# Kernel optimization log

Measured on AMD Instinct MI355X. Metric: run time of the kernel, lower is better.

## Reference

```python
import jax, jax.numpy as jnp
import numpy as np

N, D, C, E = 100000, 128, 16, 1000000
NUM_LAYERS, ALPHA = 5, 0.5
EPS_COS, EPS_LN = 1e-8, 1e-5


def setup_inputs() -> dict:
    key = jax.random.key(0)
    ks = jax.random.split(key, 10)
    inp = {
        'features': jax.random.normal(ks[0], (N, D), jnp.float32),
        'init_logits': jax.random.uniform(ks[1], (N, C), jnp.float32),
        'W': jax.random.normal(ks[2], (D, D), jnp.float32) * (1.0 / np.sqrt(D)),
        'b': jnp.zeros((D,), jnp.float32),
        'ln_gamma': jnp.ones((D,), jnp.float32),
        'ln_beta': jnp.zeros((D,), jnp.float32),
        'ew_connect': jnp.ones((1,), jnp.float32),
        'ew_decorate': jnp.ones((1,), jnp.float32),
        'ew_next': jnp.ones((1,), jnp.float32),
    }
    names = ['src_connect', 'dst_connect', 'src_decorate', 'dst_decorate', 'src_next', 'dst_next']
    for i, nm in enumerate(names):
        inp[nm] = jax.random.randint(ks[4 + (i % 6)] if False else jax.random.fold_in(ks[3], i), (E,), 0, N, jnp.int32)
    return inp


def _label_prop(features, init_logits, W, b, ln_gamma, ln_beta, ews, edges):
    # feature_transform: Linear -> LayerNorm -> ReLU (Dropout is identity in eval)
    h = features @ W.T + b
    mu = jnp.mean(h, axis=-1, keepdims=True)
    var = jnp.mean(jnp.square(h - mu), axis=-1, keepdims=True)
    h = (h - mu) * jax.lax.rsqrt(var + EPS_LN) * ln_gamma + ln_beta
    h = jax.nn.relu(h)
    # per-node L2-normalized features for cosine similarity (eps-clamped like F.cosine_similarity)
    nrm = jnp.maximum(jnp.linalg.norm(h, axis=-1), EPS_COS)
    hn = h / nrm[:, None]
    # per-edge scalar weights are fixed across layers: sigmoid(ew) * cos(src, dst)
    edge_w = []
    for ew, (src, dst) in zip(ews, edges):
        sim = jnp.sum(hn[src] * hn[dst], axis=-1)  # [E]
        edge_w.append(jax.nn.sigmoid(ew[0]) * sim)
    n_nodes = init_logits.shape[0]
    cur = init_logits
    for _ in range(NUM_LAYERS):
        next_logits = jnp.zeros_like(cur)
        total_w = jnp.zeros((n_nodes,), cur.dtype)
        for w, (src, dst) in zip(edge_w, edges):
            next_logits = next_logits.at[src].add(w[:, None] * cur[dst])
            total_w = total_w.at[src].add(w)
        pos = total_w > 0
        denom = jnp.where(pos, total_w, 1.0)[:, None]
        next_logits = jnp.where(pos[:, None], next_logits / denom, next_logits)
        cur = ALPHA * next_logits + (1.0 - ALPHA) * init_logits
    return cur


def reference(features, init_logits, W, b, ln_gamma, ln_beta, ew_connect, ew_decorate, ew_next,
              src_connect, dst_connect, src_decorate, dst_decorate, src_next, dst_next):
    ews = [ew_connect, ew_decorate, ew_next]
    edges = [(src_connect, dst_connect), (src_decorate, dst_decorate), (src_next, dst_next)]
    return _label_prop(features, init_logits, W, b, ln_gamma, ln_beta, ews, edges)
```

## Files before the change

### kernel.cpp

```cpp
#include <hip/hip_runtime.h>
#include <hip/hip_fp8.h>
#include <math.h>

#define DD 128
#define CC 16
#define ALPHA_ 0.5f
#define EPS_LN 1e-5f
#define EPS_COS 1e-8f

typedef _Float16 h2 __attribute__((ext_vector_type(2)));
typedef _Float16 h4 __attribute__((ext_vector_type(4)));
typedef _Float16 f16x8 __attribute__((ext_vector_type(8)));
typedef float f32x4 __attribute__((ext_vector_type(4)));
typedef long lx2 __attribute__((ext_vector_type(2)));

__device__ __forceinline__ unsigned pk_fp8x4(float v0, float v1, float v2, float v3) {
#if __has_builtin(__builtin_amdgcn_cvt_pk_fp8_f32)
    int u = 0;
    u = __builtin_amdgcn_cvt_pk_fp8_f32(v0, v1, u, false);
    u = __builtin_amdgcn_cvt_pk_fp8_f32(v2, v3, u, true);
    return (unsigned)u;
#else
    __hip_fp8_e4m3 a(v0), b(v1), c(v2), d(v3);
    return (unsigned)a.__x | ((unsigned)b.__x << 8)
         | ((unsigned)c.__x << 16) | ((unsigned)d.__x << 24);
#endif
}

__global__ __launch_bounds__(256, 2) void ft_mfma_kernel(
    const float* __restrict__ feat, const float* __restrict__ W,
    const float* __restrict__ bias, const float* __restrict__ gamma,
    const float* __restrict__ beta, unsigned* __restrict__ hn8, int N)
{
    const int lane = threadIdx.x & 63;
    const int c16  = lane & 15;
    const int g    = lane >> 4;
    const int wv   = (blockIdx.x * (int)blockDim.x + (int)threadIdx.x) >> 6;
    const int nwv  = ((int)gridDim.x * (int)blockDim.x) >> 6;

    f16x8 wf[8][4];
#pragma unroll
    for (int jt = 0; jt < 8; ++jt) {
        const float* wr = W + (size_t)(jt * 16 + c16) * 128 + g * 8;
#pragma unroll
        for (int s = 0; s < 4; ++s) {
            float4 lo = *(const float4*)(wr + s * 32);
            float4 hi = *(const float4*)(wr + s * 32 + 4);
            f16x8 f;
            f[0] = (_Float16)lo.x; f[1] = (_Float16)lo.y;
            f[2] = (_Float16)lo.z; f[3] = (_Float16)lo.w;
            f[4] = (_Float16)hi.x; f[5] = (_Float16)hi.y;
            f[6] = (_Float16)hi.z; f[7] = (_Float16)hi.w;
            wf[jt][s] = f;
        }
    }

    const int ntiles = (N + 15) >> 4;
    for (int t = wv; t < ntiles; t += nwv) {
        const int i = (t << 4) + c16;
        const float* fr = feat + (size_t)min(i, N - 1) * 128 + g * 8;
        f16x8 bf[4];
#pragma unroll
        for (int s = 0; s < 4; ++s) {
            float4 lo = *(const float4*)(fr + s * 32);
            float4 hi = *(const float4*)(fr + s * 32 + 4);
            f16x8 f;
            f[0] = (_Float16)lo.x; f[1] = (_Float16)lo.y;
            f[2] = (_Float16)lo.z; f[3] = (_Float16)lo.w;
            f[4] = (_Float16)hi.x; f[5] = (_Float16)hi.y;
            f[6] = (_Float16)hi.z; f[7] = (_Float16)hi.w;
            bf[s] = f;
        }

        f32x4 acc[8] = {};
#pragma unroll
        for (int s = 0; s < 4; ++s)
#pragma unroll
            for (int jt = 0; jt < 8; ++jt)
                acc[jt] = __builtin_amdgcn_mfma_f32_16x16x32_f16(
                    wf[jt][s], bf[s], acc[jt], 0, 0, 0);

        float s1 = 0.f, s2 = 0.f;
#pragma unroll
        for (int jt = 0; jt < 8; ++jt) {
            float4 bb = ((const float4*)bias)[jt * 4 + g];
            float h0 = acc[jt][0] + bb.x, h1 = acc[jt][1] + bb.y;
            float h2_ = acc[jt][2] + bb.z, h3 = acc[jt][3] + bb.w;
            acc[jt][0] = h0; acc[jt][1] = h1; acc[jt][2] = h2_; acc[jt][3] = h3;
            s1 += h0 + h1 + h2_ + h3;
            s2 += h0 * h0 + h1 * h1 + h2_ * h2_ + h3 * h3;
        }
        s1 += __shfl_xor(s1, 16); s1 += __shfl_xor(s1, 32);
        s2 += __shfl_xor(s2, 16); s2 += __shfl_xor(s2, 32);
        float mu   = s1 * (1.f / 128.f);
        float var  = s2 * (1.f / 128.f) - mu * mu;
        float rstd = rsqrtf(var + EPS_LN);

        float nsq = 0.f;
#pragma unroll
        for (int jt = 0; jt < 8; ++jt) {
            float4 gg = ((const float4*)gamma)[jt * 4 + g];
            float4 be = ((const float4*)beta)[jt * 4 + g];
            float v0 = fmaxf((acc[jt][0] - mu) * rstd * gg.x + be.x, 0.f);
            float v1 = fmaxf((acc[jt][1] - mu) * rstd * gg.y + be.y, 0.f);
            float v2 = fmaxf((acc[jt][2] - mu) * rstd * gg.z + be.z, 0.f);
            float v3 = fmaxf((acc[jt][3] - mu) * rstd * gg.w + be.w, 0.f);
            acc[jt][0] = v0; acc[jt][1] = v1; acc[jt][2] = v2; acc[jt][3] = v3;
            nsq += v0 * v0 + v1 * v1 + v2 * v2 + v3 * v3;
        }
        nsq += __shfl_xor(nsq, 16); nsq += __shfl_xor(nsq, 32);
        float inv = 1.f / fmaxf(sqrtf(nsq), EPS_COS);

        if (i < N) {
#pragma unroll
            for (int jt = 0; jt < 8; ++jt) {
                hn8[(size_t)i * 32 + jt * 4 + g] =
                    pk_fp8x4(acc[jt][0] * inv, acc[jt][1] * inv,
                             acc[jt][2] * inv, acc[jt][3] * inv);
            }
        }
    }
}

__global__ void bcount_kernel(const int* __restrict__ s0, const int* __restrict__ s1,
                              const int* __restrict__ s2, int* __restrict__ gcnt,
                              int E, int NB)
{
    __shared__ int cnt[512];
    const int tid = threadIdx.x;
    for (int i = tid; i < NB; i += 256) cnt[i] = 0;
    __syncthreads();
    const int tot = 3 * E;
    const int chunk = (tot + gridDim.x - 1) / gridDim.x;
    const int lo = blockIdx.x * chunk, hi = min(lo + chunk, tot);
    for (int i = lo + tid; i < hi; i += 256) {
        int src = (i < E) ? s0[i] : (i < 2 * E) ? s1[i - E] : s2[i - 2 * E];
        atomicAdd(&cnt[src >> 8], 1);
    }
    __syncthreads();
    for (int i = tid; i < NB; i += 256)
        if (cnt[i]) atomicAdd(&gcnt[i], cnt[i]);
}

__global__ void bscan_kernel(const int* __restrict__ gcnt, int* __restrict__ bbase,
                             int* __restrict__ gcur, int NB, int totE)
{
    __shared__ int wsum[4];
    const int t = threadIdx.x;
    const int lane = t & 63;
    int a0 = (2 * t     < NB) ? gcnt[2 * t]     : 0;
    int a1 = (2 * t + 1 < NB) ? gcnt[2 * t + 1] : 0;
    int ts = a0 + a1;
    int v = ts;
#pragma unroll
    for (int m = 1; m <= 32; m <<= 1) {
        int u = __shfl_up(v, m);
        if (lane >= m) v += u;
    }
    if (lane == 63) wsum[t >> 6] = v;
    __syncthreads();
    int woff = 0;
    for (int w = 0; w < (t >> 6); ++w) woff += wsum[w];
    int excl = woff + v - ts;
    if (2 * t < NB)     { bbase[2 * t]     = excl;      gcur[2 * t]     = excl; }
    if (2 * t + 1 < NB) { bbase[2 * t + 1] = excl + a0; gcur[2 * t + 1] = excl + a0; }
    if (t == 0) bbase[NB] = totE;
}

__global__ void bpart_kernel(
    const int* __restrict__ s0, const int* __restrict__ d0,
    const int* __restrict__ s1, const int* __restrict__ d1,
    const int* __restrict__ s2, const int* __restrict__ d2,
    int* __restrict__ gcur, unsigned* __restrict__ stage, int E, int NB)
{
    __shared__ int cnt[512];
    __shared__ int rbase[512];
    const int tid = threadIdx.x;
    for (int i = tid; i < NB; i += 256) cnt[i] = 0;
    __syncthreads();
    const int tot = 3 * E;
    const int chunk = (tot + gridDim.x - 1) / gridDim.x;
    const int lo = blockIdx.x * chunk, hi = min(lo + chunk, tot);
    for (int i = lo + tid; i < hi; i += 256) {
        int src = (i < E) ? s0[i] : (i < 2 * E) ? s1[i - E] : s2[i - 2 * E];
        atomicAdd(&cnt[src >> 8], 1);
    }
    __syncthreads();
    for (int i = tid; i < NB; i += 256) {
        int c = cnt[i];
        rbase[i] = c ? atomicAdd(&gcur[i], c) : 0;
        cnt[i] = 0;
    }
    __syncthreads();
    for (int i = lo + tid; i < hi; i += 256) {
        int src, dst, cls;
        if (i < E)          { src = s0[i];         dst = d0[i];         cls = 0; }
        else if (i < 2 * E) { src = s1[i - E];     dst = d1[i - E];     cls = 1; }
        else                { src = s2[i - 2 * E]; dst = d2[i - 2 * E]; cls = 2; }
        int b = src >> 8;
        int pos = rbase[b] + atomicAdd(&cnt[b], 1);
        stage[pos] = (unsigned)dst | ((unsigned)cls << 17) | ((unsigned)(src & 255) << 19);
    }
}

__global__ void csrfin_kernel(const unsigned* __restrict__ stage,
                              const int* __restrict__ bbase,
                              int* __restrict__ row_ptr, int* __restrict__ dstc_csr,
                              int N, int totE)
{
    __shared__ int cnt[256];
    __shared__ int wsum[4];
    const int b = blockIdx.x;
    const int t = threadIdx.x;
    const int lane = t & 63;
    const int lo = b << 8;
    const int base = bbase[b];
    const int m = bbase[b + 1] - base;

    cnt[t] = 0;
    __syncthreads();
    for (int i = t; i < m; i += 256)
        atomicAdd(&cnt[(stage[base + i] >> 19) & 255], 1);
    __syncthreads();
    int c = cnt[t];
    int v = c;
#pragma unroll
    for (int mm = 1; mm <= 32; mm <<= 1) {
        int u = __shfl_up(v, mm);
        if (lane >= mm) v += u;
    }
    if (lane == 63) wsum[t >> 6] = v;
    __syncthreads();
    int woff = 0;
    for (int w = 0; w < (t >> 6); ++w) woff += wsum[w];
    int excl = woff + v - c;
    if (lo + t < N) row_ptr[lo + t] = base + excl;
    if (b == 0 && t == 0) row_ptr[N] = totE;
    __syncthreads();
    cnt[t] = base + excl;
    __syncthreads();
    for (int i = t; i < m; i += 256) {
        unsigned v2 = stage[base + i];
        int pos = atomicAdd(&cnt[(v2 >> 19) & 255], 1);
        dstc_csr[pos] = (int)(v2 & 0x1FFFF) | (int)(((v2 >> 17) & 3) << 24);
    }
}

__global__ void node_sim_kernel(const unsigned char* __restrict__ hn8,
    const int* __restrict__ row_ptr, const int* __restrict__ dstc_csr,
    const float* __restrict__ ew0, const float* __restrict__ ew1,
    const float* __restrict__ ew2, unsigned* __restrict__ wq_csr,
    float* __restrict__ scl, int N)
{
    const int gtid = blockIdx.x * blockDim.x + threadIdx.x;
    const int lane = threadIdx.x & 63;
    const int c16  = lane & 15;
    const int g    = lane >> 4;
    const int wv   = gtid >> 6;
    const int nwv  = (gridDim.x * blockDim.x) >> 6;
    const float sg0 = 1.f / (1.f + expf(-ew0[0]));
    const float sg1 = 1.f / (1.f + expf(-ew1[0]));
    const float sg2 = 1.f / (1.f + expf(-ew2[0]));
    const bool writer = ((c16 >> 2) == g);

    for (int n = wv; n < N; n += nwv) {
        const int beg = row_ptr[n], end = row_ptr[n + 1];
        const int deg = end - beg;
        if (deg == 0) { if (lane == 0) scl[n] = ALPHA_; continue; }

        const unsigned char* sp = hn8 + (size_t)n * 128 + g * 16;
        lx2 B0 = *(const lx2*)sp;
        lx2 B1 = *(const lx2*)(sp + 64);

        float total = 0.f;
        const int nb = (deg + 15) >> 4;
        for (int kb = 0; kb < nb; ++kb) {
            const int ebase = beg + (kb << 4);
            const int rem = end - ebase;
            int vv = (c16 < rem) ? dstc_csr[ebase + c16] : 0;
            int dl = (c16 < rem) ? (vv & 0x1FFFF) : n;
            const unsigned char* rp = hn8 + (size_t)dl * 128 + g * 16;
            lx2 A0 = *(const lx2*)rp;
            lx2 A1 = *(const lx2*)(rp + 64);

            f32x4 acc = {0.f, 0.f, 0.f, 0.f};
            acc = __builtin_amdgcn_mfma_f32_16x16x32_fp8_fp8(A0[0], B0[0], acc, 0, 0, 0);
            acc = __builtin_amdgcn_mfma_f32_16x16x32_fp8_fp8(A0[1], B0[1], acc, 0, 0, 0);
            acc = __builtin_amdgcn_mfma_f32_16x16x32_fp8_fp8(A1[0], B1[0], acc, 0, 0, 0);
            acc = __builtin_amdgcn_mfma_f32_16x16x32_fp8_fp8(A1[1], B1[1], acc, 0, 0, 0);

            float w4[4];
#pragma unroll
            for (int j = 0; j < 4; ++j) {
                int ej = (g << 2) + j;
                int vj = __shfl(vv, ej);
                int cls = (vj >> 24) & 3;
                float sgc = (cls == 0) ? sg0 : (cls == 1) ? sg1 : sg2;
                float wj = sgc * acc[j];
                w4[j] = wj;
                if (ej < rem) total += wj;
            }
            if (writer && c16 < rem) {
                int j4 = c16 & 3;
                float ws = (j4 == 0) ? w4[0] : (j4 == 1) ? w4[1]
                         : (j4 == 2) ? w4[2] : w4[3];
                int q = (int)(ws * 16000.f + ((ws >= 0.f) ? 0.5f : -0.5f)) + 16384;
                q = min(max(q, 0), 32767);
                wq_csr[ebase + c16] = ((unsigned)vv & 0x1FFFFu)
                                    | ((unsigned)q << 17);
            }
        }
        total += __shfl_xor(total, 16);
        total += __shfl_xor(total, 32);
        if (lane == 0)
            scl[n] = ALPHA_ * ((total > 0.f) ? 1.f / total : 1.f);
    }
}

__global__ void cvt_kernel(const float* __restrict__ init,
                           _Float16* __restrict__ outh, int M4)
{
    int i = blockIdx.x * blockDim.x + threadIdx.x;
    int stride = gridDim.x * blockDim.x;
    for (; i < M4; i += stride) {
        float4 v = ((const float4*)init)[i];
        h4 o;
        o[0] = (_Float16)v.x; o[1] = (_Float16)v.y;
        o[2] = (_Float16)v.z; o[3] = (_Float16)v.w;
        ((h4*)outh)[i] = o;
    }
}

template<bool LAST>
__global__ void prop_kernel(const int* __restrict__ row_ptr,
    const unsigned* __restrict__ wq_csr, const float* __restrict__ scl,
    const _Float16* __restrict__ cur, const _Float16* __restrict__ inith,
    float* __restrict__ out32, _Float16* __restrict__ out16, int N)
{
    const int gtid = blockIdx.x * blockDim.x + threadIdx.x;
    const int lane = threadIdx.x & 63;
    const int sg   = lane >> 2;
    const int c4   = lane & 3;
    const int wv   = gtid >> 6;
    const int nwv  = (gridDim.x * blockDim.x) >> 6;
    const float dq = 1.f / 16000.f;
    for (int n = wv; n < N; n += nwv) {
        int beg = row_ptr[n], end = row_ptr[n + 1];
        float a0 = 0.f, a1 = 0.f, a2 = 0.f, a3 = 0.f;
#pragma unroll 2
        for (int e = beg + sg; e < end; e += 16) {
            unsigned u = wq_csr[e];
            int d = (int)(u & 0x1FFFFu);
            float w = (float)((int)(u >> 17) - 16384) * dq;
            h4 cv = *(const h4*)&cur[(size_t)d * 16 + c4 * 4];
            a0 += w * (float)cv[0];
            a1 += w * (float)cv[1];
            a2 += w * (float)cv[2];
            a3 += w * (float)cv[3];
        }
#pragma unroll
        for (int m = 4; m <= 32; m <<= 1) {
            a0 += __shfl_xor(a0, m);
            a1 += __shfl_xor(a1, m);
            a2 += __shfl_xor(a2, m);
            a3 += __shfl_xor(a3, m);
        }
        if (sg == 0) {
            float sc = scl[n];
            h4 iv = *(const h4*)&inith[(size_t)n * 16 + c4 * 4];
            float r0 = sc * a0 + (1.f - ALPHA_) * (float)iv[0];
            float r1 = sc * a1 + (1.f - ALPHA_) * (float)iv[1];
            float r2 = sc * a2 + (1.f - ALPHA_) * (float)iv[2];
            float r3 = sc * a3 + (1.f - ALPHA_) * (float)iv[3];
            if (LAST) {
                float4 st; st.x = r0; st.y = r1; st.z = r2; st.w = r3;
                *(float4*)&out32[(size_t)n * 16 + c4 * 4] = st;
            } else {
                h4 st;
                st[0] = (_Float16)r0; st[1] = (_Float16)r1;
                st[2] = (_Float16)r2; st[3] = (_Float16)r3;
                *(h4*)&out16[(size_t)n * 16 + c4 * 4] = st;
            }
        }
    }
}

extern "C" void kernel_launch(void* const* d_in, const int* in_sizes, int n_in,
                              void* d_out, int out_size, void* d_ws, size_t ws_size,
                              hipStream_t stream)
{
    const float* feat  = (const float*)d_in[0];
    const float* initl = (const float*)d_in[1];
    const float* W     = (const float*)d_in[2];
    const float* b     = (const float*)d_in[3];
    const float* gam   = (const float*)d_in[4];
    const float* bet   = (const float*)d_in[5];
    const float* ew0   = (const float*)d_in[6];
    const float* ew1   = (const float*)d_in[7];
    const float* ew2   = (const float*)d_in[8];
    const int* s0  = (const int*)d_in[9];
    const int* dd0 = (const int*)d_in[10];
    const int* s1  = (const int*)d_in[11];
    const int* dd1 = (const int*)d_in[12];
    const int* s2  = (const int*)d_in[13];
    const int* dd2 = (const int*)d_in[14];

    const int N = in_sizes[0] / DD;
    const int E = in_sizes[9];
    const int totE = 3 * E;
    const int NB = (N + 255) >> 8;
    float* out = (float*)d_out;

    char* ws = (char*)d_ws;
    size_t off = 0;
    auto alloc = [&](size_t bytes) -> void* {
        void* p = ws + off;
        off += (bytes + 255) & ~(size_t)255;
        return p;
    };
    unsigned*  hn8     = (unsigned*)alloc((size_t)N * DD);
    int*       gcnt    = (int*)alloc((size_t)(NB + 1) * 4);
    int*       bbase   = (int*)alloc((size_t)(NB + 1) * 4);
    int*       gcur    = (int*)alloc((size_t)(NB + 1) * 4);
    int*       row_ptr = (int*)alloc((size_t)(N + 1) * 4);
    unsigned*  stage   = (unsigned*)alloc((size_t)totE * 4);
    int*       dstc_csr= (int*)alloc((size_t)totE * 4);
    unsigned*  wq_csr  = (unsigned*)alloc((size_t)totE * 4);
    float*     scl     = (float*)alloc((size_t)N * 4);
    _Float16*  inith   = (_Float16*)alloc((size_t)N * CC * 2);
    _Float16*  curA    = (_Float16*)alloc((size_t)N * CC * 2);
    _Float16*  curB    = (_Float16*)alloc((size_t)N * CC * 2);

    ft_mfma_kernel<<<512, 256, 0, stream>>>(feat, W, b, gam, bet, hn8, N);

    hipMemsetAsync(gcnt, 0, (size_t)NB * 4, stream);
    bcount_kernel<<<NB, 256, 0, stream>>>(s0, s1, s2, gcnt, E, NB);
    bscan_kernel<<<1, 256, 0, stream>>>(gcnt, bbase, gcur, NB, totE);
    bpart_kernel<<<NB, 256, 0, stream>>>(s0, dd0, s1, dd1, s2, dd2,
                                         gcur, stage, E, NB);
    csrfin_kernel<<<NB, 256, 0, stream>>>(stage, bbase, row_ptr, dstc_csr, N, totE);

    const int wblk = (N * 64 + 255) / 256;
    node_sim_kernel<<<wblk, 256, 0, stream>>>((const unsigned char*)hn8,
                                              row_ptr, dstc_csr,
                                              ew0, ew1, ew2, wq_csr, scl, N);

    cvt_kernel<<<256, 256, 0, stream>>>(initl, inith, N * CC / 4);
    const _Float16* cs = inith;
    _Float16* bufs[2] = { curA, curB };
    for (int layer = 0; layer < 4; ++layer) {
        _Float16* dst = bufs[layer & 1];
        prop_kernel<false><<<wblk, 256, 0, stream>>>(row_ptr, wq_csr, scl,
                                                     cs, inith, nullptr, dst, N);
        cs = dst;
    }
    prop_kernel<true><<<wblk, 256, 0, stream>>>(row_ptr, wq_csr, scl,
                                                cs, inith, out, nullptr, N);
}
```

Measured before the change: 386.0 us.

## Fuse first propagation layer into edge-similarity kernel

The node similarity kernel now also gathers the fp16 initial logits of each neighbour and accumulates the first layer's weighted sum, writing layer-1 output directly. This removes one full prop_kernel pass over the CSR (re-reading weights and gathering neighbour logits). The similarity-to-lane mapping was rewritten so each lane owns one edge's weight, adding shuffle reductions. The first layer now uses unquantized float weights, unlike later layers, which slightly changes numerics.

```diff
diff --git a/kernel.cpp b/kernel.cpp
--- a/kernel.cpp
+++ b/kernel.cpp
@@ -8,8 +8,8 @@
 #define EPS_LN 1e-5f
 #define EPS_COS 1e-8f
 
-typedef _Float16 h2 __attribute__((ext_vector_type(2)));
 typedef _Float16 h4 __attribute__((ext_vector_type(4)));
+typedef _Float16 h8 __attribute__((ext_vector_type(8)));
 typedef _Float16 f16x8 __attribute__((ext_vector_type(8)));
 typedef float f32x4 __attribute__((ext_vector_type(4)));
 typedef long lx2 __attribute__((ext_vector_type(2)));
@@ -250,7 +250,8 @@
     const int* __restrict__ row_ptr, const int* __restrict__ dstc_csr,
     const float* __restrict__ ew0, const float* __restrict__ ew1,
     const float* __restrict__ ew2, unsigned* __restrict__ wq_csr,
-    float* __restrict__ scl, int N)
+    float* __restrict__ scl, const _Float16* __restrict__ inith,
+    _Float16* __restrict__ out1, int N)
 {
     const int gtid = blockIdx.x * blockDim.x + threadIdx.x;
     const int lane = threadIdx.x & 63;
@@ -261,18 +262,31 @@
     const float sg0 = 1.f / (1.f + expf(-ew0[0]));
     const float sg1 = 1.f / (1.f + expf(-ew1[0]));
     const float sg2 = 1.f / (1.f + expf(-ew2[0]));
-    const bool writer = ((c16 >> 2) == g);
+    const int srcl = ((c16 >> 2) << 4) | c16;
+    const int j4   = c16 & 3;
 
     for (int n = wv; n < N; n += nwv) {
         const int beg = row_ptr[n], end = row_ptr[n + 1];
         const int deg = end - beg;
-        if (deg == 0) { if (lane == 0) scl[n] = ALPHA_; continue; }
+        if (deg == 0) {
+            if (lane == 0) scl[n] = ALPHA_;
+            if (c16 == 0) {
+                h4 ivn = *(const h4*)&inith[(size_t)n * 16 + g * 4];
+                h4 st;
+#pragma unroll
+                for (int k = 0; k < 4; ++k)
+                    st[k] = (_Float16)((1.f - ALPHA_) * (float)ivn[k]);
+                *(h4*)&out1[(size_t)n * 16 + g * 4] = st;
+            }
+            continue;
+        }
 
         const unsigned char* sp = hn8 + (size_t)n * 128 + g * 16;
         lx2 B0 = *(const lx2*)sp;
         lx2 B1 = *(const lx2*)(sp + 64);
 
         float total = 0.f;
+        float p1[4] = {0.f, 0.f, 0.f, 0.f};
         const int nb = (deg + 15) >> 4;
         for (int kb = 0; kb < nb; ++kb) {
             const int ebase = beg + (kb << 4);
@@ -282,6 +296,7 @@
             const unsigned char* rp = hn8 + (size_t)dl * 128 + g * 16;
             lx2 A0 = *(const lx2*)rp;
             lx2 A1 = *(const lx2*)(rp + 64);
+            h4 ivd = *(const h4*)&inith[(size_t)dl * 16 + g * 4];
 
             f32x4 acc = {0.f, 0.f, 0.f, 0.f};
             acc = __builtin_amdgcn_mfma_f32_16x16x32_fp8_fp8(A0[0], B0[0], acc, 0, 0, 0);
@@ -289,31 +304,48 @@
             acc = __builtin_amdgcn_mfma_f32_16x16x32_fp8_fp8(A1[0], B1[0], acc, 0, 0, 0);
             acc = __builtin_amdgcn_mfma_f32_16x16x32_fp8_fp8(A1[1], B1[1], acc, 0, 0, 0);
 
-            float w4[4];
-#pragma unroll
-            for (int j = 0; j < 4; ++j) {
-                int ej = (g << 2) + j;
-                int vj = __shfl(vv, ej);
-                int cls = (vj >> 24) & 3;
-                float sgc = (cls == 0) ? sg0 : (cls == 1) ? sg1 : sg2;
-                float wj = sgc * acc[j];
-                w4[j] = wj;
-                if (ej < rem) total += wj;
+            float a01  = (j4 & 1) ? acc[1] : acc[0];
+            float a23  = (j4 & 1) ? acc[3] : acc[2];
+            float asel = (j4 & 2) ? a23 : a01;
+            float mysim = __shfl(asel, srcl);
+
+            int cls = (vv >> 24) & 3;
+            float sgc = (cls == 0) ? sg0 : (cls == 1) ? sg1 : sg2;
+            float w = sgc * mysim;
+            if (c16 < rem) {
+                total += w;
+#pragma unroll
+                for (int k = 0; k < 4; ++k) p1[k] += w * (float)ivd[k];
             }
-            if (writer && c16 < rem) {
-                int j4 = c16 & 3;
-                float ws = (j4 == 0) ? w4[0] : (j4 == 1) ? w4[1]
-                         : (j4 == 2) ? w4[2] : w4[3];
-                int q = (int)(ws * 16000.f + ((ws >= 0.f) ? 0.5f : -0.5f)) + 16384;
+
+            if (g == 0 && c16 < rem) {
+                int q = (int)(w * 16000.f + ((w >= 0.f) ? 0.5f : -0.5f)) + 16384;
                 q = min(max(q, 0), 32767);
                 wq_csr[ebase + c16] = ((unsigned)vv & 0x1FFFFu)
                                     | ((unsigned)q << 17);
             }
         }
-        total += __shfl_xor(total, 16);
-        total += __shfl_xor(total, 32);
-        if (lane == 0)
-            scl[n] = ALPHA_ * ((total > 0.f) ? 1.f / total : 1.f);
+        total += __shfl_xor(total, 1);
+        total += __shfl_xor(total, 2);
+        total += __shfl_xor(total, 4);
+        total += __shfl_xor(total, 8);
+#pragma unroll
+        for (int k = 0; k < 4; ++k) {
+            p1[k] += __shfl_xor(p1[k], 1);
+            p1[k] += __shfl_xor(p1[k], 2);
+            p1[k] += __shfl_xor(p1[k], 4);
+            p1[k] += __shfl_xor(p1[k], 8);
+        }
+        float s = ALPHA_ * ((total > 0.f) ? 1.f / total : 1.f);
+        if (lane == 0) scl[n] = s;
+        if (c16 == 0) {
+            h4 ivn = *(const h4*)&inith[(size_t)n * 16 + g * 4];
+            h4 st;
+#pragma unroll
+            for (int k = 0; k < 4; ++k)
+                st[k] = (_Float16)(s * p1[k] + (1.f - ALPHA_) * (float)ivn[k]);
+            *(h4*)&out1[(size_t)n * 16 + g * 4] = st;
+        }
     }
 }
 
@@ -440,15 +472,17 @@
                                          gcur, stage, E, NB);
     csrfin_kernel<<<NB, 256, 0, stream>>>(stage, bbase, row_ptr, dstc_csr, N, totE);
 
+    cvt_kernel<<<256, 256, 0, stream>>>(initl, inith, N * CC / 4);
+
     const int wblk = (N * 64 + 255) / 256;
     node_sim_kernel<<<wblk, 256, 0, stream>>>((const unsigned char*)hn8,
                                               row_ptr, dstc_csr,
-                                              ew0, ew1, ew2, wq_csr, scl, N);
-
-    cvt_kernel<<<256, 256, 0, stream>>>(initl, inith, N * CC / 4);
-    const _Float16* cs = inith;
-    _Float16* bufs[2] = { curA, curB };
-    for (int layer = 0; layer < 4; ++layer) {
+                                              ew0, ew1, ew2, wq_csr, scl,
+                                              inith, curA, N);
+
+    const _Float16* cs = curA;
+    _Float16* bufs[2] = { curB, curA };
+    for (int layer = 0; layer < 3; ++layer) {
         _Float16* dst = bufs[layer & 1];
         prop_kernel<false><<<wblk, 256, 0, stream>>>(row_ptr, wq_csr, scl,
                                                      cs, inith, nullptr, dst, N);
```

Result: faster. 372.5 us (-3.5%).
